# Kernel optimization log

Hardware: AMD Instinct MI355X
Metric: run time of the kernel (lower is better)

The kernel has to match this reference:

```python
import jax, jax.numpy as jnp
import numpy as np
from jax.ops import segment_sum, segment_max

ALPHA = 0.01  # leaky relu slope

def _cmul(a, b):
    # complex multiply on last-axis (re, im) pairs
    re = a[..., 0] * b[..., 0] - a[..., 1] * b[..., 1]
    im = a[..., 0] * b[..., 1] + a[..., 1] * b[..., 0]
    return jnp.stack((re, im), axis=-1)

def setup_inputs() -> dict:
    key = jax.random.key(0)
    ks = jax.random.split(key, 8)
    N, D, M, E, L, H, R, FH = 50000, 64, 3, 100000, 4, 8, 5, 128
    return {
        "features": jax.random.normal(ks[0], (N, D), jnp.float32),
        "attn1_w": jax.random.normal(ks[1], (M, H, D), jnp.float32) * 0.1,
        "attn2":   jax.random.normal(ks[2], (M, H, D), jnp.float32) * 0.1,
        "r_vec":   jax.random.normal(ks[3], (R, D // 2, 2), jnp.float32),
        "proj_w1": jax.random.normal(ks[4], (FH, H * D), jnp.float32) * 0.05,
        "proj_b1": jnp.zeros((FH,), jnp.float32),
        "proj_w2": jax.random.normal(ks[5], (1, FH), jnp.float32) * 0.1,
        "inst":    jax.random.randint(ks[6], (M, E, L), 0, N),
        "etypes":  jax.random.randint(ks[7], (M, L - 1), 0, 2 * R, dtype=jnp.int32),
    }

def reference(features, attn1_w, attn2, r_vec, proj_w1, proj_b1, proj_w2, inst, etypes):
    N, D = features.shape
    M, E, L = inst.shape
    H = attn1_w.shape[1]
    # --- conjugate-augmented, L2-normalized relation rotations ([2R, D/2, 2]) ---
    rn = r_vec / jnp.linalg.norm(r_vec, axis=2, keepdims=True)
    conj = rn * jnp.array([1.0, -1.0], rn.dtype)
    r_full = jnp.stack((rn, conj), axis=1).reshape(2 * r_vec.shape[0], r_vec.shape[1], 2)

    node_embs = []  # per-metapath [N, H*D]
    for m in range(M):
        # SemanticEncoder: gather + rotation recurrence + mean over path positions
        edata = features[inst[m]]                       # [E, L, D]
        edc = edata.reshape(E, L, D // 2, 2)
        # final_r_vec: backward cumulative complex product; position L-1 = identity
        ident = jnp.concatenate(
            [jnp.ones((D // 2, 1), edata.dtype), jnp.zeros((D // 2, 1), edata.dtype)], axis=-1)
        fr = [None] * L
        fr[L - 1] = ident
        for i in range(L - 2, -1, -1):
            fr[i] = _cmul(fr[i + 1], r_full[etypes[m, i]])
        fr = jnp.stack(fr, axis=0)                      # [L, D/2, 2]
        rotated = _cmul(edc, fr[None])                  # [E, L, D/2, 2] (pos L-1 rotated by identity)
        me = rotated.reshape(E, L, D).mean(axis=1)      # metapath embedding [E, D]

        # MessageAggregator: GAT-style segment softmax over instances per dst node
        dst = inst[m, :, 0]                             # [E]
        a1 = features[dst] @ attn1_w[m].T               # [E, H]
        a2 = jnp.einsum('ed,hd->eh', me, attn2[m])      # [E, H]
        a = jax.nn.leaky_relu(a1 + a2, ALPHA)           # [E, H]
        amax = segment_max(a, dst, num_segments=N)      # [N, H]
        amax = jnp.where(jnp.isfinite(amax), amax, 0.0)
        ex = jnp.exp(a - amax[dst])                     # [E, H]
        den = segment_sum(ex, dst, num_segments=N)      # [N, H]
        attn = ex / jnp.where(den[dst] > 0, den[dst], 1.0)
        agg = segment_sum(attn[:, :, None] * me[:, None, :], dst, num_segments=N)  # [N, H, D]
        node_embs.append(jax.nn.elu(agg).reshape(N, H * D))

    # Subgraph_Fusion: semantic attention over metapaths
    z = jnp.stack(node_embs, axis=1)                    # [N, M, H*D]
    w = jnp.tanh(z @ proj_w1.T + proj_b1) @ proj_w2.T   # [N, M, 1]
    beta = jax.nn.softmax(w.mean(axis=0), axis=0)       # [M, 1]
    out = (beta[None] * z).sum(axis=1)                  # [N, H*D]
    return out
```

## Files before the change

kernel.cpp:

```cpp
#include <hip/hip_runtime.h>
#include <hip/hip_bf16.h>
#include <hip/hip_fp16.h>
#include <math.h>

#define NN 50000
#define DD 64
#define MM 3
#define EE 100000
#define LL 4
#define HH 8
#define FHH 128
#define HD 512
#define NROWS (NN*MM)
#define LRELU_ALPHA 0.01f

#define WSUM_BINS 256
#define WSUM_SZ (MM*WSUM_BINS)
#define BINS (MM*NN)
#define NBLK ((BINS + 1023)/1024)
#define GT_TILE 224

#define FCVT_B 3125
#define CW1_B  64
#define UGEN_B 3
#define HISTG  392
#define HIST_B (HISTG*MM)
#define PREP_B (FCVT_B + CW1_B + UGEN_B + HIST_B + 1)

#define GT_B   (224*MM)
#define MID_B  (GT_B + NBLK)

#define SCAT_B (HISTG*MM)
#define SEGC_B ((BINS + 255)/256)
#define SCT_B  (SCAT_B + SEGC_B)

#define OFF_ZB    0
#define OFF_WSUM  (NROWS*HD/2)
#define OFF_BETA  (OFF_WSUM + WSUM_SZ)
#define OFF_W1BF  (OFF_BETA + 16)
#define OFF_WU    (OFF_W1BF + 32768)
#define OFF_FRS   (OFF_WU + 6144)
#define OFF_GT    (OFF_FRS + 768)
#define OFF_INTS  (OFF_GT + MM*NN*32)
#define IOFF_CNT    0
#define IOFF_CURSOR (IOFF_CNT + BINS)
#define IOFF_PART   (IOFF_CURSOR + BINS)
#define IOFF_BSUM   (IOFF_PART + BINS)
#define IOFF_BTOP   (IOFF_BSUM + 256)
#define IOFF_SEGC   (IOFF_BTOP + 256)
#define IOFF_REC    (IOFF_SEGC + 2*BINS)
#define INTS_END    (IOFF_REC + 4*MM*EE)
#define OFF_F16   (OFF_INTS + INTS_END)

typedef short v8s __attribute__((ext_vector_type(8)));
typedef float v4f __attribute__((ext_vector_type(4)));

__device__ __forceinline__ float elu_f(float x) {
    return x > 0.f ? x : (__expf(x) - 1.f);
}

__device__ __forceinline__ float tanh_fast(float x) {
    float e = __expf(2.f * x);
    return 1.f - 2.f / (e + 1.f);
}

__device__ __forceinline__ unsigned int pk_bf16x2(float x, float y) {
    float2 f2; f2.x = x; f2.y = y;
    __hip_bfloat162 h = __float22bfloat162_rn(f2);
    union { __hip_bfloat162 h; unsigned int u; } cv;
    cv.h = h;
    return cv.u;
}

__device__ __forceinline__ unsigned int pk_h2(float x, float y) {
    __half2 h = __floats2half2_rn(x, y);
    union { __half2 h; unsigned int u; } cv;
    cv.h = h;
    return cv.u;
}

__device__ __forceinline__ float bf_lo(unsigned int u) {
    union { unsigned int x; float f; } c; c.x = u << 16; return c.f;
}
__device__ __forceinline__ float bf_hi(unsigned int u) {
    union { unsigned int x; float f; } c; c.x = u & 0xffff0000u; return c.f;
}

__device__ __forceinline__ __half2 u2h(unsigned int u) {
    union { unsigned int x; __half2 h; } c; c.x = u; return c.h;
}
__device__ __forceinline__ unsigned int h2u(__half2 h) {
    union { __half2 h; unsigned int x; } c; c.h = h; return c.x;
}
__device__ __forceinline__ unsigned int swp(unsigned int u) {
    return (u >> 16) | (u << 16);
}

__device__ __forceinline__ void build_frs(
    float frs[LL][DD/2][2], const float* r_vec, const int* etypes, int m, int t)
{
    if (t < DD/2) {
        float cr = 1.f, ci = 0.f;
        frs[LL-1][t][0] = 1.f; frs[LL-1][t][1] = 0.f;
        for (int i = LL-2; i >= 0; --i) {
            int et = etypes[m*(LL-1) + i];
            float rr = r_vec[((et>>1)*(DD/2) + t)*2 + 0];
            float ri = r_vec[((et>>1)*(DD/2) + t)*2 + 1];
            float inv = rsqrtf(rr*rr + ri*ri);
            rr *= inv; ri *= inv;
            if (et & 1) ri = -ri;
            float nr = cr*rr - ci*ri;
            float ni = cr*ri + ci*rr;
            cr = nr; ci = ni;
            frs[i][t][0] = cr; frs[i][t][1] = ci;
        }
    }
}

__global__ __launch_bounds__(256) void prep_kernel(
    const float* __restrict__ features, ushort* __restrict__ f16,
    const float* __restrict__ w1, ushort* __restrict__ w1bf,
    const float* __restrict__ r_vec, const int* __restrict__ etypes,
    const float* __restrict__ attn1_w, const float* __restrict__ attn2,
    float* __restrict__ Wu, unsigned int* __restrict__ frs_h,
    const int* __restrict__ inst, int* __restrict__ cnt,
    float* __restrict__ wsum)
{
    const int b = blockIdx.x;
    const int t = threadIdx.x;
    if (b < FCVT_B) {
        int i = b*256 + t;
        float4 v = ((const float4*)features)[i];
        ((uint2*)f16)[i] = make_uint2(pk_h2(v.x, v.y), pk_h2(v.z, v.w));
    } else if (b < FCVT_B + CW1_B) {
        int i = (b - FCVT_B)*256 + t;
        float4 v = ((const float4*)w1)[i];
        uint2 p; p.x = pk_bf16x2(v.x, v.y); p.y = pk_bf16x2(v.z, v.w);
        ((uint2*)w1bf)[i] = p;
    } else if (b < FCVT_B + CW1_B + UGEN_B) {
        const int m = b - (FCVT_B + CW1_B);
        __shared__ float frs[LL][DD/2][2];
        build_frs(frs, r_vec, etypes, m, t);
        __syncthreads();
        if (t < 32) {
            unsigned int vals[8];
            #pragma unroll
            for (int l = 0; l < LL; ++l) {
                float fr = 0.25f * frs[l][t][0];
                float fi = 0.25f * frs[l][t][1];
                vals[2*l+0] = pk_h2(fr, fr);
                vals[2*l+1] = pk_h2(-fi, fi);
            }
            uint4* dst = (uint4*)frs_h + (m*32 + t)*2;
            dst[0] = make_uint4(vals[0], vals[1], vals[2], vals[3]);
            dst[1] = make_uint4(vals[4], vals[5], vals[6], vals[7]);
        }
        for (int idx = t; idx < 32*64; idx += 256) {
            int j = idx >> 6, d = idx & 63, p = d >> 1;
            int l = (j < 8) ? 0 : (j >> 3);
            int h = j & 7;
            float fr = frs[l][p][0], fi = frs[l][p][1];
            float w2r = attn2[m*HD + h*DD + 2*p];
            float w2i = attn2[m*HD + h*DD + 2*p + 1];
            float u = (d & 1) ? (fr*w2i - fi*w2r) : (fr*w2r + fi*w2i);
            float val = 0.25f * u + ((j < 8) ? attn1_w[m*HD + h*DD + d] : 0.f);
            Wu[(m*32 + j)*64 + d] = val;
        }
    } else if (b < FCVT_B + CW1_B + UGEN_B + HIST_B) {
        int idx = b - (FCVT_B + CW1_B + UGEN_B);
        int m = idx / HISTG;
        int e = (idx - m*HISTG)*256 + t;
        if (e < EE) {
            int dst = inst[((size_t)m*EE + e)*LL];
            atomicAdd(&cnt[m*NN + dst], 1);
        }
    } else {
        for (int i = t; i < WSUM_SZ; i += 256) wsum[i] = 0.f;
    }
}

__global__ __launch_bounds__(256) void mid_kernel(
    const float* __restrict__ features,
    const float* __restrict__ Wu,
    float* __restrict__ gt,
    const int* __restrict__ cnt,
    int* __restrict__ part, int* __restrict__ bsum)
{
    __shared__ float xs[GT_TILE*65];
    __shared__ int sd[256];
    const int b = blockIdx.x;
    const int t = threadIdx.x;
    if (b < GT_B) {
        const int m = b / 224;
        const int node0 = (b - m*224) * GT_TILE;
        #pragma unroll
        for (int i = 0; i < 14; ++i) {
            int idx = t + 256*i;
            int r = idx >> 4, c4 = idx & 15;
            int gr = node0 + r;
            float4 v = make_float4(0.f,0.f,0.f,0.f);
            if (gr < NN) v = ((const float4*)features)[gr*16 + c4];
            float* dst = &xs[r*65 + c4*4];
            dst[0]=v.x; dst[1]=v.y; dst[2]=v.z; dst[3]=v.w;
        }
        __syncthreads();
        if (t >= GT_TILE) return;
        int node = node0 + t;
        float acc[32];
        #pragma unroll
        for (int j=0;j<32;++j) acc[j]=0.f;
        const float* Wm = Wu + m*2048;
        for (int d = 0; d < 64; ++d) {
            float x = xs[t*65 + d];
            #pragma unroll
            for (int j = 0; j < 32; ++j)
                acc[j] += x * Wm[j*64 + d];
        }
        if (node < NN) {
            float* o = gt + ((size_t)m*NN + node)*32;
            #pragma unroll
            for (int j4 = 0; j4 < 8; ++j4) {
                float4 v; v.x=acc[j4*4]; v.y=acc[j4*4+1]; v.z=acc[j4*4+2]; v.w=acc[j4*4+3];
                ((float4*)o)[j4] = v;
            }
        }
    } else {
        const int bb = b - GT_B;
        const int base = bb*1024 + t*4;
        int v0=0,v1=0,v2=0,v3=0;
        if (base+3 < BINS) {
            int4 v = *(const int4*)&cnt[base];
            v0=v.x; v1=v.y; v2=v.z; v3=v.w;
        } else {
            if (base+0 < BINS) v0 = cnt[base+0];
            if (base+1 < BINS) v1 = cnt[base+1];
            if (base+2 < BINS) v2 = cnt[base+2];
            if (base+3 < BINS) v3 = cnt[base+3];
        }
        int tot = v0+v1+v2+v3;
        sd[t] = tot; __syncthreads();
        #pragma unroll
        for (int off = 1; off < 256; off <<= 1) {
            int val = (t >= off) ? sd[t-off] : 0;
            __syncthreads();
            sd[t] += val;
            __syncthreads();
        }
        int excl = sd[t] - tot;
        if (base+0 < BINS) part[base+0] = excl;
        if (base+1 < BINS) part[base+1] = excl + v0;
        if (base+2 < BINS) part[base+2] = excl + v0 + v1;
        if (base+3 < BINS) part[base+3] = excl + v0 + v1 + v2;
        if (t == 255) bsum[bb] = sd[255];
    }
}

__global__ __launch_bounds__(256) void scan_tops_kernel(
    const int* __restrict__ bsum, int* __restrict__ btop)
{
    __shared__ int sd[256];
    const int t = threadIdx.x;
    int v = (t < NBLK) ? bsum[t] : 0;
    sd[t] = v; __syncthreads();
    #pragma unroll
    for (int off = 1; off < 256; off <<= 1) {
        int val = (t >= off) ? sd[t-off] : 0;
        __syncthreads();
        sd[t] += val;
        __syncthreads();
    }
    if (t < NBLK) btop[t] = sd[t] - v;
}

__global__ __launch_bounds__(256) void scat_kernel(
    const int4* __restrict__ inst4, const int* __restrict__ part,
    const int* __restrict__ btop, int* __restrict__ cursor,
    int4* __restrict__ rec, const int* __restrict__ cnt,
    int2* __restrict__ segc)
{
    const int b = blockIdx.x;
    const int t = threadIdx.x;
    if (b < SCAT_B) {
        int m = b / HISTG;
        int e = (b - m*HISTG)*256 + t;
        if (e >= EE) return;
        int4 v = inst4[(size_t)m*EE + e];
        int bin = m*NN + v.x;
        int pos = part[bin] + btop[bin >> 10] + atomicAdd(&cursor[bin], 1);
        rec[pos] = make_int4(v.y, v.z, v.w, 0);
    } else {
        int i = (b - SCAT_B)*256 + t;
        if (i < BINS)
            segc[i] = make_int2(part[i] + btop[i >> 10], cnt[i]);
    }
}

__global__ __launch_bounds__(256) void node_kernel(
    const unsigned int* __restrict__ f16u,
    const unsigned int* __restrict__ frs_h,
    const int4*  __restrict__ rec4,
    const int2*  __restrict__ segc,
    const float* __restrict__ gt,
    ushort* __restrict__ Zb)
{
    const int m = blockIdx.y;
    const int t = threadIdx.x;
    const int lane = t & 63;
    const int hl   = lane & 31;
    const int half = lane >> 5;
    const int wid  = t >> 6;
    const int node = blockIdx.x*4 + wid;

    const int bin = m*NN + node;
    ushort* zrow = Zb + ((size_t)node*MM + m)*HD;
    const int2 sc = segc[bin];
    const int start = sc.x, ecnt = sc.y;
    if (ecnt == 0) {
        ((uint4*)zrow)[lane] = make_uint4(0u,0u,0u,0u);
        return;
    }

    const uint4* fh = (const uint4*)frs_h + ((size_t)(m*32 + hl))*2;
    const uint4 ca = fh[0], cb = fh[1];

    const unsigned int ux0 = f16u[(size_t)node*32 + hl];
    const __half2 me0 = __hfma2(u2h(swp(ux0)), u2h(ca.y),
                                __hmul2(u2h(ux0), u2h(ca.x)));

    const float c0 = (hl < HH) ? gt[(size_t)bin*32 + hl] : 0.f;
    const int lsel = hl >> 3;
    const bool gm = (hl >= 8);
    const float* gtm = gt + (size_t)m*NN*32;

    __half2 acc[HH];
    #pragma unroll
    for (int h = 0; h < HH; ++h) acc[h] = u2h(0u);
    float den = 0.f;

    for (int q = 0; q < ecnt; q += 2) {
        int myq = q + half;
        bool valid = (myq < ecnt);
        int qq = valid ? myq : (ecnt - 1);
        int4 r = rec4[start + qq];
        int i1 = r.x, i2 = r.y, i3 = r.z;

        int idxg = (lsel == 1) ? i1 : ((lsel == 2) ? i2 : i3);
        float gv = 0.f;
        if (gm) gv = gtm[(size_t)idxg*32 + hl];

        unsigned int u1 = f16u[(size_t)i1*32 + hl];
        unsigned int u2 = f16u[(size_t)i2*32 + hl];
        unsigned int u3 = f16u[(size_t)i3*32 + hl];

        gv += __shfl_xor(gv, 16);
        gv += __shfl_xor(gv, 8);

        __half2 me = me0;
        me = __hfma2(u2h(u1), u2h(ca.z), me);
        me = __hfma2(u2h(swp(u1)), u2h(ca.w), me);
        me = __hfma2(u2h(u2), u2h(cb.x), me);
        me = __hfma2(u2h(swp(u2)), u2h(cb.y), me);
        me = __hfma2(u2h(u3), u2h(cb.z), me);
        me = __hfma2(u2h(swp(u3)), u2h(cb.w), me);

        float a = c0 + gv;
        a = a > 0.f ? a : LRELU_ALPHA*a;
        float ex = valid ? __expf(a) : 0.f;
        den += ex;
        unsigned int exu = h2u(__float2half2_rn(ex));

        #pragma unroll
        for (int h = 0; h < HH; ++h) {
            unsigned int eu = __shfl(exu, (lane & 32) + h);
            acc[h] = __hfma2(u2h(eu), me, acc[h]);
        }
    }

    #pragma unroll
    for (int h = 0; h < HH; ++h) {
        unsigned int au = __shfl_xor(h2u(acc[h]), 32);
        acc[h] = __hadd2(acc[h], u2h(au));
    }
    den += __shfl_xor(den, 32);

    const int hbase = half ? 4 : 0;
    #pragma unroll
    for (int hh = 0; hh < 4; ++hh) {
        int h = hbase + hh;
        unsigned int sel = half ? h2u(acc[hh+4]) : h2u(acc[hh]);
        float dh = __shfl(den, h);
        float inv = __builtin_amdgcn_rcpf(dh);
        float2 v = __half22float2(u2h(sel));
        float vr = elu_f(v.x * inv);
        float vi = elu_f(v.y * inv);
        ((unsigned int*)zrow)[h*32 + hl] = pk_bf16x2(vr, vi);
    }
}


__global__ __launch_bounds__(256,3) void wproj_kernel(
    const ushort* __restrict__ Zb,
    const ushort* __restrict__ w1bf,
    const float* __restrict__ b1,
    const float* __restrict__ w2,
    float* __restrict__ wsum)
{
    __shared__ ushort As[128*72];
    __shared__ ushort Bs[128*72];
    __shared__ float wacc[MM];
    const int t = threadIdx.x;
    const int row0 = blockIdx.x * 128;
    if (t < MM) wacc[t] = 0.f;
    const int lane = t & 63;
    const int wid  = t >> 6;
    const int ln   = lane & 15;
    const int quad = lane >> 4;
    const int wr   = wid >> 1;
    const int wc   = wid & 1;

    v4f acc[4][4];
    #pragma unroll
    for (int i=0;i<4;++i)
        #pragma unroll
        for (int j=0;j<4;++j)
            acc[i][j] = (v4f){0.f,0.f,0.f,0.f};

    const uint4* zb4 = (const uint4*)Zb;
    const uint4* wb4 = (const uint4*)w1bf;

    for (int kt = 0; kt < 8; ++kt) {
        __syncthreads();
        #pragma unroll
        for (int i = 0; i < 4; ++i) {
            int idx = t + 256*i;
            int r = idx >> 3, k8 = idx & 7;
            int gr = row0 + r;
            uint4 v = make_uint4(0u,0u,0u,0u);
            if (gr < NROWS) v = zb4[(size_t)gr*64 + kt*8 + k8];
            *(uint4*)&As[r*72 + k8*8] = v;
        }
        #pragma unroll
        for (int i = 0; i < 4; ++i) {
            int idx = t + 256*i;
            int f = idx >> 3, k8 = idx & 7;
            uint4 v = wb4[f*64 + kt*8 + k8];
            *(uint4*)&Bs[f*72 + k8*8] = v;
        }
        __syncthreads();
        #pragma unroll
        for (int kk = 0; kk < 2; ++kk) {
            v8s a[4], b[4];
            #pragma unroll
            for (int i=0;i<4;++i)
                a[i] = *(const v8s*)&As[(wr*64 + i*16 + ln)*72 + kk*32 + quad*8];
            #pragma unroll
            for (int j=0;j<4;++j)
                b[j] = *(const v8s*)&Bs[(wc*64 + j*16 + ln)*72 + kk*32 + quad*8];
            #pragma unroll
            for (int i=0;i<4;++i)
                #pragma unroll
                for (int j=0;j<4;++j)
                    acc[i][j] = __builtin_amdgcn_mfma_f32_16x16x32_bf16(
                        a[i], b[j], acc[i][j], 0, 0, 0);
        }
    }

    float b1v[4], w2v[4];
    #pragma unroll
    for (int j=0;j<4;++j) {
        int col = wc*64 + j*16 + ln;
        b1v[j] = b1[col];
        w2v[j] = w2[col];
    }
    #pragma unroll
    for (int i=0;i<4;++i) {
        #pragma unroll
        for (int reg=0;reg<4;++reg) {
            float s = 0.f;
            #pragma unroll
            for (int j=0;j<4;++j)
                s += tanh_fast(acc[i][j][reg] + b1v[j]) * w2v[j];
            s += __shfl_xor(s, 1);
            s += __shfl_xor(s, 2);
            s += __shfl_xor(s, 4);
            s += __shfl_xor(s, 8);
            int grow = row0 + wr*64 + i*16 + quad*4 + reg;
            if (ln == 0 && grow < NROWS)
                atomicAdd(&wacc[grow % MM], s);
        }
    }
    __syncthreads();
    if (t < MM)
        atomicAdd(&wsum[t*WSUM_BINS + (blockIdx.x & (WSUM_BINS-1))], wacc[t]);
}

__global__ void beta_kernel(const float* __restrict__ wsum, float* __restrict__ beta)
{
    __shared__ float sm[MM];
    int t = threadIdx.x;
    if (t < MM) {
        float s = 0.f;
        for (int i = 0; i < WSUM_BINS; ++i) s += wsum[t*WSUM_BINS + i];
        sm[t] = s / (float)NN;
    }
    __syncthreads();
    if (t < MM) {
        float a = sm[0], b = sm[1], c = sm[2];
        float mx = fmaxf(a, fmaxf(b, c));
        float e0 = __expf(a-mx), e1 = __expf(b-mx), e2 = __expf(c-mx);
        float tot = e0+e1+e2;
        float mine = (t==0?e0:(t==1?e1:e2));
        beta[t] = mine/tot;
    }
}

__global__ __launch_bounds__(256) void out_kernel(
    const ushort* __restrict__ Zb, const float* __restrict__ beta,
    float* __restrict__ out)
{
    int i = blockIdx.x*256 + threadIdx.x;
    int n  = i >> 6;
    int jj = i & 63;
    float b0 = beta[0], b1v = beta[1], b2 = beta[2];
    const uint4* zb4 = (const uint4*)Zb;
    uint4 v0 = zb4[((size_t)n*MM + 0)*64 + jj];
    uint4 v1 = zb4[((size_t)n*MM + 1)*64 + jj];
    uint4 v2 = zb4[((size_t)n*MM + 2)*64 + jj];
    float o[8];
    o[0] = b0*bf_lo(v0.x) + b1v*bf_lo(v1.x) + b2*bf_lo(v2.x);
    o[1] = b0*bf_hi(v0.x) + b1v*bf_hi(v1.x) + b2*bf_hi(v2.x);
    o[2] = b0*bf_lo(v0.y) + b1v*bf_lo(v1.y) + b2*bf_lo(v2.y);
    o[3] = b0*bf_hi(v0.y) + b1v*bf_hi(v1.y) + b2*bf_hi(v2.y);
    o[4] = b0*bf_lo(v0.z) + b1v*bf_lo(v1.z) + b2*bf_lo(v2.z);
    o[5] = b0*bf_hi(v0.z) + b1v*bf_hi(v1.z) + b2*bf_hi(v2.z);
    o[6] = b0*bf_lo(v0.w) + b1v*bf_lo(v1.w) + b2*bf_lo(v2.w);
    o[7] = b0*bf_hi(v0.w) + b1v*bf_hi(v1.w) + b2*bf_hi(v2.w);
    float4* op = (float4*)(out + (size_t)n*HD + jj*8);
    op[0] = make_float4(o[0],o[1],o[2],o[3]);
    op[1] = make_float4(o[4],o[5],o[6],o[7]);
}

extern "C" void kernel_launch(void* const* d_in, const int* in_sizes, int n_in,
                              void* d_out, int out_size, void* d_ws, size_t ws_size,
                              hipStream_t stream) {
    const float* features = (const float*)d_in[0];
    const float* attn1_w  = (const float*)d_in[1];
    const float* attn2    = (const float*)d_in[2];
    const float* r_vec    = (const float*)d_in[3];
    const float* proj_w1  = (const float*)d_in[4];
    const float* proj_b1  = (const float*)d_in[5];
    const float* proj_w2  = (const float*)d_in[6];
    const int*   inst     = (const int*)d_in[7];
    const int*   etypes   = (const int*)d_in[8];
    float* out = (float*)d_out;

    float* ws    = (float*)d_ws;
    ushort* Zb   = (ushort*)(ws + OFF_ZB);
    float* wsum  = ws + OFF_WSUM;
    float* beta  = ws + OFF_BETA;
    ushort* w1bf = (ushort*)(ws + OFF_W1BF);
    float* Wu    = ws + OFF_WU;
    unsigned int* frs_h = (unsigned int*)(ws + OFF_FRS);
    float* gt    = ws + OFF_GT;
    int* ints    = (int*)(ws + OFF_INTS);
    int* cnt     = ints + IOFF_CNT;
    int* cursor  = ints + IOFF_CURSOR;
    int* part    = ints + IOFF_PART;
    int* bsum    = ints + IOFF_BSUM;
    int* btop    = ints + IOFF_BTOP;
    int2* segc   = (int2*)(ints + IOFF_SEGC);
    int4* rec4   = (int4*)(ints + IOFF_REC);
    ushort* f16  = (ushort*)(ws + OFF_F16);

    hipMemsetAsync(cnt, 0, (size_t)2*BINS*sizeof(int), stream);

    prep_kernel<<<PREP_B, 256, 0, stream>>>(
        features, f16, proj_w1, w1bf, r_vec, etypes, attn1_w, attn2,
        Wu, frs_h, inst, cnt, wsum);
    mid_kernel<<<MID_B, 256, 0, stream>>>(features, Wu, gt, cnt, part, bsum);
    scan_tops_kernel<<<1, 256, 0, stream>>>(bsum, btop);
    scat_kernel<<<SCT_B, 256, 0, stream>>>(
        (const int4*)inst, part, btop, cursor, rec4, cnt, segc);
    node_kernel<<<dim3(NN/4, MM), 256, 0, stream>>>(
        (const unsigned int*)f16, frs_h, rec4, segc, gt, Zb);
    wproj_kernel<<<(NROWS + 127)/128, 256, 0, stream>>>(Zb, w1bf, proj_b1, proj_w2, wsum);
    beta_kernel<<<1, 64, 0, stream>>>(wsum, beta);
    out_kernel<<<NN*64/256, 256, 0, stream>>>(Zb, beta, out);
}
```

Measured before the change: 354.3 us.

## Inline first two edge records per segment and use op_sel packed FMAs

The scatter kernel now writes the first two instances of each destination bin into a 32-byte per-bin segment record that also holds the start and count. The node kernel reads this record and processes the first edge pair without touching the rec4 array, which removes one dependent load for the common low-degree case. The half-precision complex rotation and the per-head accumulation now use inline v_pk_fma_f16 with op_sel and op_sel_hi, so the separate swap and broadcast instructions go away. Blocks shrink from 256 to 128 threads. The per-bin segment storage grows fourfold, and the scatter kernel adds extra scattered stores.

```diff
diff --git a/kernel.cpp b/kernel.cpp
--- a/kernel.cpp
+++ b/kernel.cpp
@@ -47,8 +47,8 @@
 #define IOFF_PART   (IOFF_CURSOR + BINS)
 #define IOFF_BSUM   (IOFF_PART + BINS)
 #define IOFF_BTOP   (IOFF_BSUM + 256)
-#define IOFF_SEGC   (IOFF_BTOP + 256)
-#define IOFF_REC    (IOFF_SEGC + 2*BINS)
+#define IOFF_SEG8   (IOFF_BTOP + 256)
+#define IOFF_REC    (IOFF_SEG8 + 8*BINS)
 #define INTS_END    (IOFF_REC + 4*MM*EE)
 #define OFF_F16   (OFF_INTS + INTS_END)
 
@@ -92,8 +92,24 @@
 __device__ __forceinline__ unsigned int h2u(__half2 h) {
     union { __half2 h; unsigned int x; } c; c.h = h; return c.x;
 }
-__device__ __forceinline__ unsigned int swp(unsigned int u) {
-    return (u >> 16) | (u << 16);
+
+__device__ __forceinline__ unsigned int pk_fma(unsigned int x, unsigned int c, unsigned int a) {
+    unsigned int d;
+    asm("v_pk_fma_f16 %0, %1, %2, %3"
+        : "=v"(d) : "v"(x), "v"(c), "v"(a));
+    return d;
+}
+__device__ __forceinline__ unsigned int pk_fma_swap0(unsigned int x, unsigned int c, unsigned int a) {
+    unsigned int d;
+    asm("v_pk_fma_f16 %0, %1, %2, %3 op_sel:[1,0,0] op_sel_hi:[0,1,1]"
+        : "=v"(d) : "v"(x), "v"(c), "v"(a));
+    return d;
+}
+__device__ __forceinline__ unsigned int pk_fma_bcast0(unsigned int x, unsigned int c, unsigned int a) {
+    unsigned int d;
+    asm("v_pk_fma_f16 %0, %1, %2, %3 op_sel:[0,0,0] op_sel_hi:[0,1,1]"
+        : "=v"(d) : "v"(x), "v"(c), "v"(a));
+    return d;
 }
 
 __device__ __forceinline__ void build_frs(
@@ -276,7 +292,7 @@
     const int4* __restrict__ inst4, const int* __restrict__ part,
     const int* __restrict__ btop, int* __restrict__ cursor,
     int4* __restrict__ rec, const int* __restrict__ cnt,
-    int2* __restrict__ segc)
+    int* __restrict__ seg8)
 {
     const int b = blockIdx.x;
     const int t = threadIdx.x;
@@ -286,20 +302,25 @@
         if (e >= EE) return;
         int4 v = inst4[(size_t)m*EE + e];
         int bin = m*NN + v.x;
-        int pos = part[bin] + btop[bin >> 10] + atomicAdd(&cursor[bin], 1);
+        int c = atomicAdd(&cursor[bin], 1);
+        int pos = part[bin] + btop[bin >> 10] + c;
         rec[pos] = make_int4(v.y, v.z, v.w, 0);
+        if (c < 2) {
+            int* s = seg8 + bin*8 + 2 + c*3;
+            s[0] = v.y; s[1] = v.z; s[2] = v.w;
+        }
     } else {
         int i = (b - SCAT_B)*256 + t;
         if (i < BINS)
-            segc[i] = make_int2(part[i] + btop[i >> 10], cnt[i]);
-    }
-}
-
-__global__ __launch_bounds__(256) void node_kernel(
+            ((int2*)seg8)[i*4] = make_int2(part[i] + btop[i >> 10], cnt[i]);
+    }
+}
+
+__global__ __launch_bounds__(128) void node_kernel(
     const unsigned int* __restrict__ f16u,
     const unsigned int* __restrict__ frs_h,
     const int4*  __restrict__ rec4,
-    const int2*  __restrict__ segc,
+    const int*   __restrict__ seg8,
     const float* __restrict__ gt,
     ushort* __restrict__ Zb)
 {
@@ -309,12 +330,14 @@
     const int hl   = lane & 31;
     const int half = lane >> 5;
     const int wid  = t >> 6;
-    const int node = blockIdx.x*4 + wid;
+    const int node = blockIdx.x*2 + wid;
 
     const int bin = m*NN + node;
     ushort* zrow = Zb + ((size_t)node*MM + m)*HD;
-    const int2 sc = segc[bin];
-    const int start = sc.x, ecnt = sc.y;
+    const int4 sa = ((const int4*)seg8)[bin*2 + 0];
+    const int4 sb = ((const int4*)seg8)[bin*2 + 1];
+    const int start = __builtin_amdgcn_readfirstlane(sa.x);
+    const int ecnt  = __builtin_amdgcn_readfirstlane(sa.y);
     if (ecnt == 0) {
         ((uint4*)zrow)[lane] = make_uint4(0u,0u,0u,0u);
         return;
@@ -324,62 +347,68 @@
     const uint4 ca = fh[0], cb = fh[1];
 
     const unsigned int ux0 = f16u[(size_t)node*32 + hl];
-    const __half2 me0 = __hfma2(u2h(swp(ux0)), u2h(ca.y),
-                                __hmul2(u2h(ux0), u2h(ca.x)));
+    unsigned int me0u = h2u(__hmul2(u2h(ux0), u2h(ca.x)));
+    me0u = pk_fma_swap0(ux0, ca.y, me0u);
 
     const float c0 = (hl < HH) ? gt[(size_t)bin*32 + hl] : 0.f;
     const int lsel = hl >> 3;
     const bool gm = (hl >= 8);
     const float* gtm = gt + (size_t)m*NN*32;
 
-    __half2 acc[HH];
+    unsigned int acc[HH];
     #pragma unroll
-    for (int h = 0; h < HH; ++h) acc[h] = u2h(0u);
+    for (int h = 0; h < HH; ++h) acc[h] = 0u;
     float den = 0.f;
 
-    for (int q = 0; q < ecnt; q += 2) {
-        int myq = q + half;
-        bool valid = (myq < ecnt);
-        int qq = valid ? myq : (ecnt - 1);
-        int4 r = rec4[start + qq];
-        int i1 = r.x, i2 = r.y, i3 = r.z;
-
+    auto edge = [&](int i1, int i2, int i3, bool valid) {
         int idxg = (lsel == 1) ? i1 : ((lsel == 2) ? i2 : i3);
         float gv = 0.f;
         if (gm) gv = gtm[(size_t)idxg*32 + hl];
-
         unsigned int u1 = f16u[(size_t)i1*32 + hl];
         unsigned int u2 = f16u[(size_t)i2*32 + hl];
         unsigned int u3 = f16u[(size_t)i3*32 + hl];
-
         gv += __shfl_xor(gv, 16);
         gv += __shfl_xor(gv, 8);
-
-        __half2 me = me0;
-        me = __hfma2(u2h(u1), u2h(ca.z), me);
-        me = __hfma2(u2h(swp(u1)), u2h(ca.w), me);
-        me = __hfma2(u2h(u2), u2h(cb.x), me);
-        me = __hfma2(u2h(swp(u2)), u2h(cb.y), me);
-        me = __hfma2(u2h(u3), u2h(cb.z), me);
-        me = __hfma2(u2h(swp(u3)), u2h(cb.w), me);
-
+        unsigned int me = me0u;
+        me = pk_fma(u1, ca.z, me);
+        me = pk_fma_swap0(u1, ca.w, me);
+        me = pk_fma(u2, cb.x, me);
+        me = pk_fma_swap0(u2, cb.y, me);
+        me = pk_fma(u3, cb.z, me);
+        me = pk_fma_swap0(u3, cb.w, me);
         float a = c0 + gv;
-        a = a > 0.f ? a : LRELU_ALPHA*a;
+        a = fmaxf(a, LRELU_ALPHA*a);
         float ex = valid ? __expf(a) : 0.f;
         den += ex;
-        unsigned int exu = h2u(__float2half2_rn(ex));
-
+        unsigned int exu = (unsigned int)__half_as_ushort(__float2half(ex));
         #pragma unroll
         for (int h = 0; h < HH; ++h) {
             unsigned int eu = __shfl(exu, (lane & 32) + h);
-            acc[h] = __hfma2(u2h(eu), me, acc[h]);
+            acc[h] = pk_fma_bcast0(eu, me, acc[h]);
+        }
+    };
+
+    {
+        bool useB = (half == 1) && (ecnt >= 2);
+        int i1 = useB ? sb.y : sa.z;
+        int i2 = useB ? sb.z : sa.w;
+        int i3 = useB ? sb.w : sb.x;
+        edge(i1, i2, i3, half == 0 || ecnt >= 2);
+    }
+    if (ecnt > 2) {
+        for (int q = 2; q < ecnt; q += 2) {
+            int myq = q + half;
+            bool valid = (myq < ecnt);
+            int qq = valid ? myq : (ecnt - 1);
+            int4 r = rec4[start + qq];
+            edge(r.x, r.y, r.z, valid);
         }
     }
 
     #pragma unroll
     for (int h = 0; h < HH; ++h) {
-        unsigned int au = __shfl_xor(h2u(acc[h]), 32);
-        acc[h] = __hadd2(acc[h], u2h(au));
+        unsigned int au = __shfl_xor(acc[h], 32);
+        acc[h] = h2u(__hadd2(u2h(acc[h]), u2h(au)));
     }
     den += __shfl_xor(den, 32);
 
@@ -387,7 +416,7 @@
     #pragma unroll
     for (int hh = 0; hh < 4; ++hh) {
         int h = hbase + hh;
-        unsigned int sel = half ? h2u(acc[hh+4]) : h2u(acc[hh]);
+        unsigned int sel = half ? acc[hh+4] : acc[hh];
         float dh = __shfl(den, h);
         float inv = __builtin_amdgcn_rcpf(dh);
         float2 v = __half22float2(u2h(sel));
@@ -568,7 +597,7 @@
     int* part    = ints + IOFF_PART;
     int* bsum    = ints + IOFF_BSUM;
     int* btop    = ints + IOFF_BTOP;
-    int2* segc   = (int2*)(ints + IOFF_SEGC);
+    int* seg8    = ints + IOFF_SEG8;
     int4* rec4   = (int4*)(ints + IOFF_REC);
     ushort* f16  = (ushort*)(ws + OFF_F16);
 
@@ -580,9 +609,9 @@
     mid_kernel<<<MID_B, 256, 0, stream>>>(features, Wu, gt, cnt, part, bsum);
     scan_tops_kernel<<<1, 256, 0, stream>>>(bsum, btop);
     scat_kernel<<<SCT_B, 256, 0, stream>>>(
-        (const int4*)inst, part, btop, cursor, rec4, cnt, segc);
-    node_kernel<<<dim3(NN/4, MM), 256, 0, stream>>>(
-        (const unsigned int*)f16, frs_h, rec4, segc, gt, Zb);
+        (const int4*)inst, part, btop, cursor, rec4, cnt, seg8);
+    node_kernel<<<dim3(NN/2, MM), 128, 0, stream>>>(
+        (const unsigned int*)f16, frs_h, rec4, seg8, gt, Zb);
     wproj_kernel<<<(NROWS + 127)/128, 256, 0, stream>>>(Zb, w1bf, proj_b1, proj_w2, wsum);
     beta_kernel<<<1, 64, 0, stream>>>(wsum, beta);
     out_kernel<<<NN*64/256, 256, 0, stream>>>(Zb, beta, out);
```

Measured after the change: 357.5 us. Within noise of the previous version (+0.9%).
